# Kernel tuning notes

Measured on AMD Instinct MI355X. Metric: run time of the kernel, lower is better.

## Reference

```python
import jax, jax.numpy as jnp
import numpy as np

B, N, D_IN, D_H = 16, 8192, 64, 64
N_SUP, K_HOP = 2, 2
NUM_MAT = N_SUP * K_HOP + 1  # identity + k hops per support
D_CAT = D_IN + D_H


def setup_inputs() -> dict:
    key = jax.random.key(0)
    ks = jax.random.split(key, 6)
    inputs = jax.random.normal(ks[0], (B, N, D_IN), jnp.float32)
    states = jax.random.normal(ks[1], (B, N, D_H), jnp.float32)
    # random-walk-like supports: nonnegative, row mass ~O(1) so k-hop features stay sane
    supports = jax.random.uniform(ks[2], (N_SUP, N, N), jnp.float32) * (2.0 / N)
    W_ru = jax.random.normal(ks[3], (D_CAT * NUM_MAT, 2 * D_H), jnp.float32) * 0.02
    b_ru = jnp.ones((2 * D_H,), jnp.float32)  # bias_start=1.0
    W_c = jax.random.normal(ks[4], (D_CAT * NUM_MAT, D_H), jnp.float32) * 0.02
    b_c = jnp.zeros((D_H,), jnp.float32)
    return dict(inputs=inputs, states=states, supports=supports,
                W_ru=W_ru, b_ru=b_ru, W_c=W_c, b_c=b_c)


def _gconv(x, supports, W, b):
    # x: [B,N,D]; diffusion conv: concat [x, S x, (2 S - I applied via Chebyshev) ...]
    feats = [x]
    for i in range(N_SUP):
        s = supports[i]  # [N,N]
        x1 = jnp.einsum('nm,bmd->bnd', s, x)
        feats.append(x1)
        xk2, xk1 = x, x1
        for _ in range(2, K_HOP + 1):
            xk = 2.0 * jnp.einsum('nm,bmd->bnd', s, xk1) - xk2
            feats.append(xk)
            xk2, xk1 = xk1, xk
    h = jnp.concatenate(feats, axis=-1)  # [B,N,D*NUM_MAT]
    return jnp.einsum('bnf,fo->bno', h, W) + b


def reference(inputs, states, supports, W_ru, b_ru, W_c, b_c):
    x = jnp.concatenate([inputs, states], axis=-1)           # [B,N,D_CAT]
    ru = jax.nn.sigmoid(_gconv(x, supports, W_ru, b_ru))      # [B,N,2H]
    r, u = ru[..., :D_H], ru[..., D_H:]
    xc = jnp.concatenate([inputs, r * states], axis=-1)
    c = jnp.tanh(_gconv(xc, supports, W_c, b_c))              # [B,N,H]
    new_state = u * states + (1.0 - u) * c
    return new_state, new_state
```

## Files before the change

kernel.cpp:

```cpp
#include <hip/hip_runtime.h>
#include <math.h>

typedef unsigned short u16t;
typedef unsigned int   u32t;
using short8 = __attribute__((ext_vector_type(8))) short;
using f32x4  = __attribute__((ext_vector_type(4))) float;

#define SZ_S   67108864LL
#define SZ_F   16777216LL
#define SZ_G   8388608LL
#define OFF_S0  0LL
#define OFF_S1  67108864LL
#define OFF_XT  134217728LL
#define OFF_X10 150994944LL
#define OFF_Z0  167772160LL
#define OFF_X11 184549376LL
#define OFF_Z1  201326592LL
#define OFF_RUT 218103808LL
#define OFF_YT  234881024LL
#define OFF_Y10 243269632LL
#define OFF_ZY0 251658240LL
#define OFF_Y11 260046848LL
#define OFF_ZY1 268435456LL
#define OFF_CT  276824064LL
#define OFF_WRU 285212672LL
#define OFF_WC  285294592LL

__device__ __forceinline__ u16t f2b(float f) {
  u32t x = __float_as_uint(f);
  x += 0x7fffu + ((x >> 16) & 1u);
  return (u16t)(x >> 16);
}
__device__ __forceinline__ float b2f(u16t h) {
  return __uint_as_float(((u32t)h) << 16);
}
__device__ __forceinline__ void async16(const u16t* g, u16t* l) {
  __builtin_amdgcn_global_load_lds((const __attribute__((address_space(1))) void*)g,
                                   (__attribute__((address_space(3))) void*)l, 16, 0, 0);
}

__global__ void convert_s(const float* __restrict__ S, u16t* __restrict__ ws) {
  const long long tid = (long long)blockIdx.x * 256 + threadIdx.x;
  const float4* p = (const float4*)S;
  const float4 a = p[tid * 2];
  const float4 b = p[tid * 2 + 1];
  short8 o;
  o[0] = (short)f2b(a.x); o[1] = (short)f2b(a.y);
  o[2] = (short)f2b(a.z); o[3] = (short)f2b(a.w);
  o[4] = (short)f2b(b.x); o[5] = (short)f2b(b.y);
  o[6] = (short)f2b(b.z); o[7] = (short)f2b(b.w);
  *(short8*)&ws[OFF_S0 + tid * 8] = o;
}

__global__ void build_xt(const float* __restrict__ inputs,
                         const float* __restrict__ states,
                         u16t* __restrict__ ws) {
  __shared__ float tile[64][65];
  const int n0 = blockIdx.x * 64;
  const int half = blockIdx.y;
  const int b = blockIdx.z;
  const float* src = half ? states : inputs;
  const int t = threadIdx.x;
  const int d = t & 63, nl = t >> 6;
#pragma unroll
  for (int p = 0; p < 16; ++p) {
    const int n = p * 4 + nl;
    tile[d][n] = src[((long long)b * 8192 + n0 + n) * 64 + d];
  }
  __syncthreads();
  const int nn = t & 63, cl = t >> 6;
#pragma unroll
  for (int p = 0; p < 16; ++p) {
    const int c = p * 4 + cl;
    ws[OFF_XT + (long long)(b * 128 + half * 64 + c) * 8192 + n0 + nn] = f2b(tile[c][nn]);
  }
}

__global__ void prep_w(const float* __restrict__ Wru, const float* __restrict__ Wc,
                       u16t* __restrict__ ws) {
  const int t = blockIdx.x * 256 + threadIdx.x;
  if (t < 81920) {
    const int o = t / 640, f = t - o * 640;
    const int feat = f >> 7, dc = f & 127;
    float v;
    switch (feat) {
      case 0:  v = Wru[dc * 128 + o] - Wru[(256 + dc) * 128 + o] - Wru[(512 + dc) * 128 + o]; break;
      case 1:  v = Wru[(128 + dc) * 128 + o]; break;
      case 2:  v = 2.f * Wru[(256 + dc) * 128 + o]; break;
      case 3:  v = Wru[(384 + dc) * 128 + o]; break;
      default: v = 2.f * Wru[(512 + dc) * 128 + o]; break;
    }
    ws[OFF_WRU + t] = f2b(v);
  } else {
    const int t2 = t - 81920;
    const int o = t2 / 640, f = t2 - o * 640;
    const int feat = f >> 7, dc = f & 127;
    float v;
    switch (feat) {
      case 0:  v = Wc[dc * 64 + o] - Wc[(256 + dc) * 64 + o] - Wc[(512 + dc) * 64 + o]; break;
      case 1:  v = Wc[(128 + dc) * 64 + o]; break;
      case 2:  v = 2.f * Wc[(256 + dc) * 64 + o]; break;
      case 3:  v = Wc[(384 + dc) * 64 + o]; break;
      default: v = 2.f * Wc[(512 + dc) * 64 + o]; break;
    }
    ws[OFF_WC + t2] = f2b(v);
  }
}

__global__ __launch_bounds__(256, 2) void gemm_bt(const u16t* __restrict__ A,
                                                  const u16t* __restrict__ S,
                                                  u16t* __restrict__ Out) {
  __shared__ __align__(16) u16t As[128 * 64];
  __shared__ __align__(16) u16t Bs[128 * 64];
  const int t = threadIdx.x;
  const int l = t & 63;
  const int w = t >> 6;
  const int m0 = blockIdx.x * 128;
  const long long r0 = (long long)blockIdx.y * 128;

  const int srow = t >> 3;
  const int schunk = ((t & 7) ^ (srow & 7)) * 8;
  const u16t* ga = A + (r0 + srow) * 8192 + schunk;
  const u16t* gb = S + (long long)(m0 + srow) * 8192 + schunk;
  u16t* la = &As[t * 8];
  u16t* lb = &Bs[t * 8];

  f32x4 acc[4][4];
#pragma unroll
  for (int i = 0; i < 4; ++i)
#pragma unroll
    for (int j = 0; j < 4; ++j) acc[i][j] = f32x4{0.f, 0.f, 0.f, 0.f};

  const int wr = (w >> 1) * 64, wm = (w & 1) * 64;
  const int lm = l & 15, lq = l >> 4;

  for (int k0 = 0; k0 < 8192; k0 += 64) {
#pragma unroll
    for (int i = 0; i < 4; ++i) {
      async16(ga + (long long)i * 32 * 8192 + k0, la + i * 2048);
      async16(gb + (long long)i * 32 * 8192 + k0, lb + i * 2048);
    }
    __syncthreads();
#pragma unroll
    for (int s = 0; s < 2; ++s) {
      short8 af[4], bf[4];
      const int ch = s * 4 + lq;
#pragma unroll
      for (int i = 0; i < 4; ++i) {
        const int mr = wr + i * 16 + lm;
        const int nr = wm + i * 16 + lm;
        af[i] = *(const short8*)&As[mr * 64 + ((ch ^ (mr & 7)) * 8)];
        bf[i] = *(const short8*)&Bs[nr * 64 + ((ch ^ (nr & 7)) * 8)];
      }
#pragma unroll
      for (int i = 0; i < 4; ++i)
#pragma unroll
        for (int j = 0; j < 4; ++j)
          acc[i][j] = __builtin_amdgcn_mfma_f32_16x16x32_bf16(af[i], bf[j], acc[i][j], 0, 0, 0);
    }
    __syncthreads();
  }
#pragma unroll
  for (int i = 0; i < 4; ++i)
#pragma unroll
    for (int j = 0; j < 4; ++j)
#pragma unroll
      for (int rr = 0; rr < 4; ++rr) {
        const long long r = r0 + wr + i * 16 + lq * 4 + rr;
        const int c = m0 + wm + j * 16 + lm;
        Out[r * 8192 + c] = f2b(acc[i][j][rr]);
      }
}

__global__ __launch_bounds__(256, 2) void proj(const u16t* __restrict__ ws_c,
                                               u16t* __restrict__ ws_m,
                                               const float* __restrict__ bias,
                                               const int variant) {
  __shared__ __align__(16) u16t As[128 * 64];
  __shared__ __align__(16) u16t Bt[128 * 72];
  const long long FOFF[5] = {OFF_XT, OFF_X10, OFF_Z0, OFF_X11, OFF_Z1};
  const long long GOFF[5] = {OFF_YT, OFF_Y10, OFF_ZY0, OFF_Y11, OFF_ZY1};
  const int t = threadIdx.x;
  const int l = t & 63;
  const int w = t >> 6;
  const int n0 = blockIdx.x * 128;
  const int b = blockIdx.y;
  const u16t* Wt = ws_c + (variant ? OFF_WC : OFF_WRU);

  const int srow = t >> 3;
  const int schunk = ((t & 7) ^ (srow & 7)) * 8;
  const int wr = (w >> 1) * 64, wm = (w & 1) * 64;
  const int lm = l & 15, lq = l >> 4;

  f32x4 acc[4][4];
#pragma unroll
  for (int i = 0; i < 4; ++i)
#pragma unroll
    for (int j = 0; j < 4; ++j) acc[i][j] = f32x4{0.f, 0.f, 0.f, 0.f};

  for (int q = 0; q < 10; ++q) {
    const int feat = q >> 1, half = q & 1;
    long long brow;
    if (variant == 0)
      brow = FOFF[feat] + (long long)(b * 128 + half * 64) * 8192;
    else
      brow = half ? (GOFF[feat] + (long long)(b * 64) * 8192)
                  : (FOFF[feat] + (long long)(b * 128) * 8192);
#pragma unroll
    for (int i = 0; i < 4; ++i)
      async16(Wt + (i * 32 + srow) * 640 + q * 64 + schunk, &As[i * 2048 + t * 8]);
    const int fr = t >> 4;
    const int noff = (t & 15) * 8;
#pragma unroll
    for (int p = 0; p < 4; ++p) {
      const int f = p * 16 + fr;
      short8 v = *(const short8*)&ws_c[brow + (long long)f * 8192 + n0 + noff];
#pragma unroll
      for (int e = 0; e < 8; ++e) Bt[(noff + e) * 72 + f] = (u16t)v[e];
    }
    __syncthreads();
#pragma unroll
    for (int s = 0; s < 2; ++s) {
      short8 af[4], bf[4];
      const int ch = s * 4 + lq;
#pragma unroll
      for (int i = 0; i < 4; ++i) {
        const int mr = wr + i * 16 + lm;
        const int nr = wm + i * 16 + lm;
        af[i] = *(const short8*)&As[mr * 64 + ((ch ^ (mr & 7)) * 8)];
        bf[i] = *(const short8*)&Bt[nr * 72 + s * 32 + lq * 8];
      }
#pragma unroll
      for (int i = 0; i < 4; ++i)
#pragma unroll
        for (int j = 0; j < 4; ++j)
          acc[i][j] = __builtin_amdgcn_mfma_f32_16x16x32_bf16(af[i], bf[j], acc[i][j], 0, 0, 0);
    }
    __syncthreads();
  }

  if (variant == 0) {
#pragma unroll
    for (int i = 0; i < 4; ++i)
#pragma unroll
      for (int j = 0; j < 4; ++j)
#pragma unroll
        for (int rr = 0; rr < 4; ++rr) {
          const int o = wr + i * 16 + lq * 4 + rr;
          const int c = n0 + wm + j * 16 + lm;
          const float x = acc[i][j][rr] + bias[o];
          const float sg = 1.f / (1.f + __expf(-x));
          ws_m[OFF_RUT + (long long)(b * 128 + o) * 8192 + c] = f2b(sg);
        }
  } else if (wr == 0) {
#pragma unroll
    for (int i = 0; i < 4; ++i)
#pragma unroll
      for (int j = 0; j < 4; ++j)
#pragma unroll
        for (int rr = 0; rr < 4; ++rr) {
          const int o = i * 16 + lq * 4 + rr;
          const int c = n0 + wm + j * 16 + lm;
          const float x = acc[i][j][rr] + bias[o];
          ws_m[OFF_CT + (long long)(b * 64 + o) * 8192 + c] = f2b(tanhf(x));
        }
  }
}

__global__ void build_y(u16t* __restrict__ ws) {
  const long long tid = (long long)blockIdx.x * 256 + threadIdx.x;
  const int ry = (int)(tid >> 10);
  const int nc = ((int)tid & 1023) * 8;
  const int b = ry >> 6, d = ry & 63;
  const short8 r8 = *(const short8*)&ws[OFF_RUT + (long long)(b * 128 + d) * 8192 + nc];
  const short8 s8 = *(const short8*)&ws[OFF_XT + (long long)(b * 128 + 64 + d) * 8192 + nc];
  short8 o;
#pragma unroll
  for (int e = 0; e < 8; ++e) o[e] = (short)f2b(b2f((u16t)r8[e]) * b2f((u16t)s8[e]));
  *(short8*)&ws[OFF_YT + (long long)ry * 8192 + nc] = o;
}

__global__ void final_out(const u16t* __restrict__ ws,
                          const float* __restrict__ states,
                          float* __restrict__ out) {
  __shared__ float lu[64][65];
  __shared__ float lc[64][65];
  const int t = threadIdx.x;
  const int b = blockIdx.y;
  const int n0 = blockIdx.x * 64;
  const int dd = t >> 3, noff = (t & 7) * 8;
#pragma unroll
  for (int p = 0; p < 2; ++p) {
    const int d = p * 32 + dd;
    short8 u8 = *(const short8*)&ws[OFF_RUT + (long long)(b * 128 + 64 + d) * 8192 + n0 + noff];
    short8 c8 = *(const short8*)&ws[OFF_CT + (long long)(b * 64 + d) * 8192 + n0 + noff];
#pragma unroll
    for (int e = 0; e < 8; ++e) {
      lu[d][noff + e] = b2f((u16t)u8[e]);
      lc[d][noff + e] = b2f((u16t)c8[e]);
    }
  }
  __syncthreads();
  const int d = t & 63, nl = t >> 6;
#pragma unroll
  for (int p = 0; p < 16; ++p) {
    const int n = p * 4 + nl;
    const long long idx = ((long long)b * 8192 + n0 + n) * 64 + d;
    const float s = states[idx];
    const float u = lu[d][n];
    const float c = lc[d][n];
    const float v = u * s + (1.f - u) * c;
    out[idx] = v;
    out[idx + 8388608] = v;
  }
}

extern "C" void kernel_launch(void* const* d_in, const int* in_sizes, int n_in,
                              void* d_out, int out_size, void* d_ws, size_t ws_size,
                              hipStream_t stream) {
  (void)in_sizes; (void)n_in; (void)out_size; (void)ws_size;
  const float* inputs   = (const float*)d_in[0];
  const float* states   = (const float*)d_in[1];
  const float* supports = (const float*)d_in[2];
  const float* Wru      = (const float*)d_in[3];
  const float* bru      = (const float*)d_in[4];
  const float* Wc       = (const float*)d_in[5];
  const float* bc       = (const float*)d_in[6];
  u16t* ws = (u16t*)d_ws;
  float* out = (float*)d_out;

  convert_s<<<65536, 256, 0, stream>>>(supports, ws);
  build_xt<<<dim3(128, 2, 16), 256, 0, stream>>>(inputs, states, ws);
  prep_w<<<480, 256, 0, stream>>>(Wru, Wc, ws);

  gemm_bt<<<dim3(64, 16), 256, 0, stream>>>(ws + OFF_XT,  ws + OFF_S0, ws + OFF_X10);
  gemm_bt<<<dim3(64, 16), 256, 0, stream>>>(ws + OFF_X10, ws + OFF_S0, ws + OFF_Z0);
  gemm_bt<<<dim3(64, 16), 256, 0, stream>>>(ws + OFF_XT,  ws + OFF_S1, ws + OFF_X11);
  gemm_bt<<<dim3(64, 16), 256, 0, stream>>>(ws + OFF_X11, ws + OFF_S1, ws + OFF_Z1);

  proj<<<dim3(64, 16), 256, 0, stream>>>(ws, ws, bru, 0);
  build_y<<<4096, 256, 0, stream>>>(ws);

  gemm_bt<<<dim3(64, 8), 256, 0, stream>>>(ws + OFF_YT,  ws + OFF_S0, ws + OFF_Y10);
  gemm_bt<<<dim3(64, 8), 256, 0, stream>>>(ws + OFF_Y10, ws + OFF_S0, ws + OFF_ZY0);
  gemm_bt<<<dim3(64, 8), 256, 0, stream>>>(ws + OFF_YT,  ws + OFF_S1, ws + OFF_Y11);
  gemm_bt<<<dim3(64, 8), 256, 0, stream>>>(ws + OFF_Y11, ws + OFF_S1, ws + OFF_ZY1);

  proj<<<dim3(64, 16), 256, 0, stream>>>(ws, ws, bc, 1);
  final_out<<<dim3(128, 16), 256, 0, stream>>>(ws, states, out);
}
```

Before: 2.503 ms.

## Replace GEMM with 256x256 double-buffered pipelined kernel batching both supports

Swaps the 128x128 single-buffered GEMM for a 256x256-tile, 512-thread kernel. It double-buffers LDS, issues async global loads in half-tiles interleaved with MFMA phases, and uses explicit barriers, waitcnts and setprio to overlap loads with compute. Two supports run in one launch via blockIdx.z, and a grouped block-id swizzle is added for L2 reuse. The aim is to hide memory latency and raise arithmetic intensity per block. The cost is heavy register use (128 accumulator floats per thread), 128KB of LDS per block, and fragile manual wait counts.

```diff
diff --git a/kernel.cpp b/kernel.cpp
--- a/kernel.cpp
+++ b/kernel.cpp
@@ -107,68 +107,136 @@
   }
 }
 
-__global__ __launch_bounds__(256, 2) void gemm_bt(const u16t* __restrict__ A,
-                                                  const u16t* __restrict__ S,
-                                                  u16t* __restrict__ Out) {
-  __shared__ __align__(16) u16t As[128 * 64];
-  __shared__ __align__(16) u16t Bs[128 * 64];
+#define STAGE(g, lb, kt, half)                                                   \
+  { const long long kk2 = (long long)(((kt) & 127) * 64);                        \
+    async16((g) + ((long long)((half) * 128 + srl)) * 8192 + kk2 + ssx,          \
+            (lb) + (half) * 8192 + sld);                                         \
+    async16((g) + ((long long)((half) * 128 + srl + 8)) * 8192 + kk2 + ssx,      \
+            (lb) + (half) * 8192 + sld + 512); }
+
+#define GRP(T, CUR)                                                              \
+  {                                                                              \
+    short8 af0[8], af1[8], bf0[4], bf1[4];                                       \
+         \
+    _Pragma("unroll") for (int mi = 0; mi < 8; ++mi) {                           \
+      af0[mi] = *(const short8*)&As[CUR][ar0 + mi * 1024];                       \
+      af1[mi] = *(const short8*)&As[CUR][ar1 + mi * 1024];                       \
+    }                                                                            \
+    _Pragma("unroll") for (int nj = 0; nj < 4; ++nj)                             \
+      bf0[nj] = *(const short8*)&Bs[CUR][br0 + nj * 1024];                       \
+    STAGE(gB, Bs[1 - (CUR)], (T) + 1, 1);                                        \
+    __builtin_amdgcn_s_barrier();                                                \
+    asm volatile("s_waitcnt lgkmcnt(0)" ::: "memory");                           \
+    __builtin_amdgcn_sched_barrier(0);                                           \
+    __builtin_amdgcn_s_setprio(1);                                               \
+    _Pragma("unroll") for (int mi = 0; mi < 8; ++mi) {                           \
+      acc[mi][0] = __builtin_amdgcn_mfma_f32_16x16x32_bf16(af0[mi], bf0[0], acc[mi][0], 0, 0, 0); \
+      acc[mi][1] = __builtin_amdgcn_mfma_f32_16x16x32_bf16(af0[mi], bf0[1], acc[mi][1], 0, 0, 0); \
+    }                                                                            \
+    __builtin_amdgcn_s_setprio(0);                                               \
+    __builtin_amdgcn_s_barrier();                                                \
+       \
+    STAGE(gA, As[CUR], (T) + 2, 0);                                              \
+    __builtin_amdgcn_s_barrier();                                                \
+    __builtin_amdgcn_s_setprio(1);                                               \
+    _Pragma("unroll") for (int mi = 0; mi < 8; ++mi) {                           \
+      acc[mi][2] = __builtin_amdgcn_mfma_f32_16x16x32_bf16(af0[mi], bf0[2], acc[mi][2], 0, 0, 0); \
+      acc[mi][3] = __builtin_amdgcn_mfma_f32_16x16x32_bf16(af0[mi], bf0[3], acc[mi][3], 0, 0, 0); \
+    }                                                                            \
+    __builtin_amdgcn_s_setprio(0);                                               \
+    __builtin_amdgcn_s_barrier();                                                \
+                       \
+    _Pragma("unroll") for (int nj = 0; nj < 4; ++nj)                             \
+      bf1[nj] = *(const short8*)&Bs[CUR][br1 + nj * 1024];                       \
+    STAGE(gA, As[CUR], (T) + 2, 1);                                              \
+    __builtin_amdgcn_s_barrier();                                                \
+    asm volatile("s_waitcnt lgkmcnt(0)" ::: "memory");                           \
+    __builtin_amdgcn_sched_barrier(0);                                           \
+    __builtin_amdgcn_s_setprio(1);                                               \
+    _Pragma("unroll") for (int mi = 0; mi < 8; ++mi) {                           \
+      acc[mi][0] = __builtin_amdgcn_mfma_f32_16x16x32_bf16(af1[mi], bf1[0], acc[mi][0], 0, 0, 0); \
+      acc[mi][1] = __builtin_amdgcn_mfma_f32_16x16x32_bf16(af1[mi], bf1[1], acc[mi][1], 0, 0, 0); \
+    }                                                                            \
+    __builtin_amdgcn_s_setprio(0);                                               \
+    __builtin_amdgcn_s_barrier();                                                \
+       \
+    STAGE(gB, Bs[CUR], (T) + 2, 0);                                              \
+    __builtin_amdgcn_s_barrier();                                                \
+    __builtin_amdgcn_s_setprio(1);                                               \
+    _Pragma("unroll") for (int mi = 0; mi < 8; ++mi) {                           \
+      acc[mi][2] = __builtin_amdgcn_mfma_f32_16x16x32_bf16(af1[mi], bf1[2], acc[mi][2], 0, 0, 0); \
+      acc[mi][3] = __builtin_amdgcn_mfma_f32_16x16x32_bf16(af1[mi], bf1[3], acc[mi][3], 0, 0, 0); \
+    }                                                                            \
+    __builtin_amdgcn_s_setprio(0);                                               \
+    asm volatile("s_waitcnt vmcnt(6)" ::: "memory");                             \
+    __builtin_amdgcn_s_barrier();                                                \
+  }
+
+__global__ __launch_bounds__(512, 2) void gemm256(const u16t* __restrict__ Aa,
+                                                  const u16t* __restrict__ Sa,
+                                                  u16t* __restrict__ Oa,
+                                                  const u16t* __restrict__ Ab,
+                                                  const u16t* __restrict__ Sb,
+                                                  u16t* __restrict__ Ob) {
+  __shared__ __align__(16) u16t As[2][16384];
+  __shared__ __align__(16) u16t Bs[2][16384];
   const int t = threadIdx.x;
   const int l = t & 63;
   const int w = t >> 6;
-  const int m0 = blockIdx.x * 128;
-  const long long r0 = (long long)blockIdx.y * 128;
-
-  const int srow = t >> 3;
-  const int schunk = ((t & 7) ^ (srow & 7)) * 8;
-  const u16t* ga = A + (r0 + srow) * 8192 + schunk;
-  const u16t* gb = S + (long long)(m0 + srow) * 8192 + schunk;
-  u16t* la = &As[t * 8];
-  u16t* lb = &Bs[t * 8];
-
-  f32x4 acc[4][4];
-#pragma unroll
-  for (int i = 0; i < 4; ++i)
+  const int id = blockIdx.y * 32 + blockIdx.x;
+  const int cpx = (gridDim.y * 32) >> 3;
+  const int swz = (id & 7) * cpx + (id >> 3);
+  const int bx = swz & 31, by = swz >> 5;
+  const long long m0 = (long long)bx * 256;
+  const long long r0 = (long long)by * 256;
+  const u16t* A = blockIdx.z ? Ab : Aa;
+  const u16t* S = blockIdx.z ? Sb : Sa;
+  u16t* Out = blockIdx.z ? Ob : Oa;
+  const u16t* gA = A + r0 * 8192;
+  const u16t* gB = S + m0 * 8192;
+
+  const int wr = (w >> 2) * 128;
+  const int wc = (w & 3) * 64;
+  const int lm = l & 15, lq = l >> 4;
+
+  const int srl = w * 16 + (l >> 3);
+  const int ssx = ((l & 7) ^ ((l >> 3) & 7)) * 8;
+  const int sld = w * 1024 + l * 8;
+
+  const int ar0 = (wr + lm) * 64 + ((lq ^ (lm & 7)) * 8);
+  const int ar1 = (wr + lm) * 64 + (((4 + lq) ^ (lm & 7)) * 8);
+  const int br0 = (wc + lm) * 64 + ((lq ^ (lm & 7)) * 8);
+  const int br1 = (wc + lm) * 64 + (((4 + lq) ^ (lm & 7)) * 8);
+
+  f32x4 acc[8][4];
+#pragma unroll
+  for (int i = 0; i < 8; ++i)
 #pragma unroll
     for (int j = 0; j < 4; ++j) acc[i][j] = f32x4{0.f, 0.f, 0.f, 0.f};
 
-  const int wr = (w >> 1) * 64, wm = (w & 1) * 64;
-  const int lm = l & 15, lq = l >> 4;
-
-  for (int k0 = 0; k0 < 8192; k0 += 64) {
-#pragma unroll
-    for (int i = 0; i < 4; ++i) {
-      async16(ga + (long long)i * 32 * 8192 + k0, la + i * 2048);
-      async16(gb + (long long)i * 32 * 8192 + k0, lb + i * 2048);
-    }
-    __syncthreads();
-#pragma unroll
-    for (int s = 0; s < 2; ++s) {
-      short8 af[4], bf[4];
-      const int ch = s * 4 + lq;
-#pragma unroll
-      for (int i = 0; i < 4; ++i) {
-        const int mr = wr + i * 16 + lm;
-        const int nr = wm + i * 16 + lm;
-        af[i] = *(const short8*)&As[mr * 64 + ((ch ^ (mr & 7)) * 8)];
-        bf[i] = *(const short8*)&Bs[nr * 64 + ((ch ^ (nr & 7)) * 8)];
-      }
-#pragma unroll
-      for (int i = 0; i < 4; ++i)
-#pragma unroll
-        for (int j = 0; j < 4; ++j)
-          acc[i][j] = __builtin_amdgcn_mfma_f32_16x16x32_bf16(af[i], bf[j], acc[i][j], 0, 0, 0);
-    }
-    __syncthreads();
-  }
-#pragma unroll
-  for (int i = 0; i < 4; ++i)
-#pragma unroll
-    for (int j = 0; j < 4; ++j)
+  STAGE(gA, As[0], 0, 0); STAGE(gA, As[0], 0, 1);
+  STAGE(gB, Bs[0], 0, 0); STAGE(gB, Bs[0], 0, 1);
+  asm volatile("s_waitcnt vmcnt(4)" ::: "memory");
+  STAGE(gA, As[1], 1, 0); STAGE(gA, As[1], 1, 1);
+  STAGE(gB, Bs[1], 1, 0);
+  asm volatile("s_waitcnt vmcnt(6)" ::: "memory");
+  __builtin_amdgcn_s_barrier();
+
+#pragma unroll 1
+  for (int T = 0; T < 128; T += 2) {
+    GRP(T, 0)
+    GRP(T + 1, 1)
+  }
+
+#pragma unroll
+  for (int mi = 0; mi < 8; ++mi)
+#pragma unroll
+    for (int nj = 0; nj < 4; ++nj)
 #pragma unroll
       for (int rr = 0; rr < 4; ++rr) {
-        const long long r = r0 + wr + i * 16 + lq * 4 + rr;
-        const int c = m0 + wm + j * 16 + lm;
-        Out[r * 8192 + c] = f2b(acc[i][j][rr]);
+        const long long r = r0 + wr + mi * 16 + lq * 4 + rr;
+        const long long c = m0 + wc + nj * 16 + lm;
+        Out[r * 8192 + c] = f2b(acc[mi][nj][rr]);
       }
 }
 
@@ -333,18 +401,18 @@
   build_xt<<<dim3(128, 2, 16), 256, 0, stream>>>(inputs, states, ws);
   prep_w<<<480, 256, 0, stream>>>(Wru, Wc, ws);
 
-  gemm_bt<<<dim3(64, 16), 256, 0, stream>>>(ws + OFF_XT,  ws + OFF_S0, ws + OFF_X10);
-  gemm_bt<<<dim3(64, 16), 256, 0, stream>>>(ws + OFF_X10, ws + OFF_S0, ws + OFF_Z0);
-  gemm_bt<<<dim3(64, 16), 256, 0, stream>>>(ws + OFF_XT,  ws + OFF_S1, ws + OFF_X11);
-  gemm_bt<<<dim3(64, 16), 256, 0, stream>>>(ws + OFF_X11, ws + OFF_S1, ws + OFF_Z1);
+  gemm256<<<dim3(32, 8, 2), 512, 0, stream>>>(ws + OFF_XT,  ws + OFF_S0, ws + OFF_X10,
+                                              ws + OFF_XT,  ws + OFF_S1, ws + OFF_X11);
+  gemm256<<<dim3(32, 8, 2), 512, 0, stream>>>(ws + OFF_X10, ws + OFF_S0, ws + OFF_Z0,
+                                              ws + OFF_X11, ws + OFF_S1, ws + OFF_Z1);
 
   proj<<<dim3(64, 16), 256, 0, stream>>>(ws, ws, bru, 0);
   build_y<<<4096, 256, 0, stream>>>(ws);
 
-  gemm_bt<<<dim3(64, 8), 256, 0, stream>>>(ws + OFF_YT,  ws + OFF_S0, ws + OFF_Y10);
-  gemm_bt<<<dim3(64, 8), 256, 0, stream>>>(ws + OFF_Y10, ws + OFF_S0, ws + OFF_ZY0);
-  gemm_bt<<<dim3(64, 8), 256, 0, stream>>>(ws + OFF_YT,  ws + OFF_S1, ws + OFF_Y11);
-  gemm_bt<<<dim3(64, 8), 256, 0, stream>>>(ws + OFF_Y11, ws + OFF_S1, ws + OFF_ZY1);
+  gemm256<<<dim3(32, 4, 2), 512, 0, stream>>>(ws + OFF_YT,  ws + OFF_S0, ws + OFF_Y10,
+                                              ws + OFF_YT,  ws + OFF_S1, ws + OFF_Y11);
+  gemm256<<<dim3(32, 4, 2), 512, 0, stream>>>(ws + OFF_Y10, ws + OFF_S0, ws + OFF_ZY0,
+                                              ws + OFF_Y11, ws + OFF_S1, ws + OFF_ZY1);
 
   proj<<<dim3(64, 16), 256, 0, stream>>>(ws, ws, bc, 1);
   final_out<<<dim3(128, 16), 256, 0, stream>>>(ws, states, out);
```

Result: faster. 2.379 ms (-5.0%).

## Replace GEMM with 256x256-tile multi-stage pipelined kernel batching both supports

Applied to the files above, without the earlier changes.

Swaps the 128x128 single-buffered GEMM for a 256x256-tile, 512-thread kernel. It uses a 4-deep LDS ring of 32-wide K slices with async prefetch three steps ahead, register double-buffering of fragments, setprio around MFMA bursts, and a block-index swizzle for L2 locality. The two independent support GEMMs per hop are merged into one launch via blockIdx.z. The aim is to hide global-load latency, raise arithmetic intensity per LDS byte, and cut launch count, at the cost of much higher register and LDS pressure (128KB LDS with 2 blocks per CU requested).

```diff
diff --git a/kernel.cpp b/kernel.cpp
--- a/kernel.cpp
+++ b/kernel.cpp
@@ -107,68 +107,116 @@
   }
 }
 
-__global__ __launch_bounds__(256, 2) void gemm_bt(const u16t* __restrict__ A,
-                                                  const u16t* __restrict__ S,
-                                                  u16t* __restrict__ Out) {
-  __shared__ __align__(16) u16t As[128 * 64];
-  __shared__ __align__(16) u16t Bs[128 * 64];
+#define STAGE_A(kt, dst)                                                        \
+  { const long long kw = (long long)(((kt) & 255) * 32);                        \
+    async16(gA + (long long)srow2 * 8192 + kw + sgc8, (dst) + sldo);            \
+    async16(gA + (long long)(srow2 + 128) * 8192 + kw + sgc8, (dst) + 4096 + sldo); }
+#define STAGE_B(kt, dst)                                                        \
+  { const long long kw = (long long)(((kt) & 255) * 32);                        \
+    async16(gB + (long long)srow2 * 8192 + kw + sgc8, (dst) + 8192 + sldo);     \
+    async16(gB + (long long)(srow2 + 128) * 8192 + kw + sgc8, (dst) + 12288 + sldo); }
+
+__global__ __launch_bounds__(512, 2) void gemm256(const u16t* __restrict__ Aa,
+                                                  const u16t* __restrict__ Sa,
+                                                  u16t* __restrict__ Oa,
+                                                  const u16t* __restrict__ Ab,
+                                                  const u16t* __restrict__ Sb,
+                                                  u16t* __restrict__ Ob) {
+  __shared__ __align__(16) u16t lds[4][16384];
   const int t = threadIdx.x;
   const int l = t & 63;
   const int w = t >> 6;
-  const int m0 = blockIdx.x * 128;
-  const long long r0 = (long long)blockIdx.y * 128;
-
-  const int srow = t >> 3;
-  const int schunk = ((t & 7) ^ (srow & 7)) * 8;
-  const u16t* ga = A + (r0 + srow) * 8192 + schunk;
-  const u16t* gb = S + (long long)(m0 + srow) * 8192 + schunk;
-  u16t* la = &As[t * 8];
-  u16t* lb = &Bs[t * 8];
-
-  f32x4 acc[4][4];
-#pragma unroll
-  for (int i = 0; i < 4; ++i)
+  const int id = blockIdx.y * 32 + blockIdx.x;
+  const int cpx = (gridDim.y * 32) >> 3;
+  const int swz = (id & 7) * cpx + (id >> 3);
+  const int bx = swz & 31, by = swz >> 5;
+  const long long m0 = (long long)bx * 256;
+  const long long r0 = (long long)by * 256;
+  const u16t* A = blockIdx.z ? Ab : Aa;
+  const u16t* S = blockIdx.z ? Sb : Sa;
+  u16t* Out = blockIdx.z ? Ob : Oa;
+  const u16t* gA = A + r0 * 8192;
+  const u16t* gB = S + m0 * 8192;
+
+  const int wr = (w >> 2) * 128;
+  const int wc = (w & 3) * 64;
+  const int lm = l & 15, lq = l >> 4;
+
+  const int srow2 = t >> 2;
+  const int sgc8 = ((t & 3) ^ ((t >> 3) & 3)) * 8;
+  const int sldo = t * 8;
+
+  const int ch8 = (lq ^ ((lm >> 1) & 3)) * 8;
+  const int aoff = (wr + lm) * 32 + ch8;
+  const int boff0 = 8192 + (wc + lm) * 32 + ch8;
+  const int boff1 = boff0 + 1024;
+
+  f32x4 acc[8][4];
+#pragma unroll
+  for (int i = 0; i < 8; ++i)
 #pragma unroll
     for (int j = 0; j < 4; ++j) acc[i][j] = f32x4{0.f, 0.f, 0.f, 0.f};
 
-  const int wr = (w >> 1) * 64, wm = (w & 1) * 64;
-  const int lm = l & 15, lq = l >> 4;
-
-  for (int k0 = 0; k0 < 8192; k0 += 64) {
-#pragma unroll
-    for (int i = 0; i < 4; ++i) {
-      async16(ga + (long long)i * 32 * 8192 + k0, la + i * 2048);
-      async16(gb + (long long)i * 32 * 8192 + k0, lb + i * 2048);
-    }
-    __syncthreads();
-#pragma unroll
-    for (int s = 0; s < 2; ++s) {
-      short8 af[4], bf[4];
-      const int ch = s * 4 + lq;
-#pragma unroll
-      for (int i = 0; i < 4; ++i) {
-        const int mr = wr + i * 16 + lm;
-        const int nr = wm + i * 16 + lm;
-        af[i] = *(const short8*)&As[mr * 64 + ((ch ^ (mr & 7)) * 8)];
-        bf[i] = *(const short8*)&Bs[nr * 64 + ((ch ^ (nr & 7)) * 8)];
-      }
-#pragma unroll
-      for (int i = 0; i < 4; ++i)
-#pragma unroll
-        for (int j = 0; j < 4; ++j)
-          acc[i][j] = __builtin_amdgcn_mfma_f32_16x16x32_bf16(af[i], bf[j], acc[i][j], 0, 0, 0);
-    }
-    __syncthreads();
-  }
-#pragma unroll
-  for (int i = 0; i < 4; ++i)
-#pragma unroll
-    for (int j = 0; j < 4; ++j)
+  STAGE_A(0, &lds[0][0]); STAGE_B(0, &lds[0][0]);
+  STAGE_A(1, &lds[1][0]); STAGE_B(1, &lds[1][0]);
+  STAGE_A(2, &lds[2][0]); STAGE_B(2, &lds[2][0]);
+  asm volatile("s_waitcnt vmcnt(4)" ::: "memory");
+  __builtin_amdgcn_s_barrier();
+
+  short8 fa[8], fb[2], ga[8], gb[2];
+  {
+    const u16t* b0 = &lds[0][0];
+#pragma unroll
+    for (int mi = 0; mi < 8; ++mi) fa[mi] = *(const short8*)&b0[aoff + mi * 512];
+#pragma unroll
+    for (int j = 0; j < 2; ++j) fb[j] = *(const short8*)&b0[boff0 + j * 512];
+  }
+
+#pragma unroll 1
+  for (int T = 0; T < 256; ++T) {
+    const u16t* bT  = &lds[T & 3][0];
+    const u16t* bT1 = &lds[(T + 1) & 3][0];
+    u16t* sD = &lds[(T + 3) & 3][0];
+    STAGE_A(T + 3, sD);
+#pragma unroll
+    for (int mi = 0; mi < 8; ++mi) ga[mi] = *(const short8*)&bT[aoff + mi * 512];
+#pragma unroll
+    for (int j = 0; j < 2; ++j) gb[j] = *(const short8*)&bT[boff1 + j * 512];
+    __builtin_amdgcn_s_barrier();
+    __builtin_amdgcn_s_setprio(1);
+#pragma unroll
+    for (int mi = 0; mi < 8; ++mi) {
+      acc[mi][0] = __builtin_amdgcn_mfma_f32_16x16x32_bf16(fa[mi], fb[0], acc[mi][0], 0, 0, 0);
+      acc[mi][1] = __builtin_amdgcn_mfma_f32_16x16x32_bf16(fa[mi], fb[1], acc[mi][1], 0, 0, 0);
+    }
+    __builtin_amdgcn_s_setprio(0);
+    __builtin_amdgcn_s_barrier();
+    STAGE_B(T + 3, sD);
+#pragma unroll
+    for (int mi = 0; mi < 8; ++mi) fa[mi] = *(const short8*)&bT1[aoff + mi * 512];
+#pragma unroll
+    for (int j = 0; j < 2; ++j) fb[j] = *(const short8*)&bT1[boff0 + j * 512];
+    __builtin_amdgcn_s_barrier();
+    __builtin_amdgcn_s_setprio(1);
+#pragma unroll
+    for (int mi = 0; mi < 8; ++mi) {
+      acc[mi][2] = __builtin_amdgcn_mfma_f32_16x16x32_bf16(ga[mi], gb[0], acc[mi][2], 0, 0, 0);
+      acc[mi][3] = __builtin_amdgcn_mfma_f32_16x16x32_bf16(ga[mi], gb[1], acc[mi][3], 0, 0, 0);
+    }
+    __builtin_amdgcn_s_setprio(0);
+    asm volatile("s_waitcnt vmcnt(4)" ::: "memory");
+    __builtin_amdgcn_s_barrier();
+  }
+
+#pragma unroll
+  for (int mi = 0; mi < 8; ++mi)
+#pragma unroll
+    for (int nj = 0; nj < 4; ++nj)
 #pragma unroll
       for (int rr = 0; rr < 4; ++rr) {
-        const long long r = r0 + wr + i * 16 + lq * 4 + rr;
-        const int c = m0 + wm + j * 16 + lm;
-        Out[r * 8192 + c] = f2b(acc[i][j][rr]);
+        const long long r = r0 + wr + mi * 16 + lq * 4 + rr;
+        const long long c = m0 + wc + nj * 16 + lm;
+        Out[r * 8192 + c] = f2b(acc[mi][nj][rr]);
       }
 }
 
@@ -333,18 +381,18 @@
   build_xt<<<dim3(128, 2, 16), 256, 0, stream>>>(inputs, states, ws);
   prep_w<<<480, 256, 0, stream>>>(Wru, Wc, ws);
 
-  gemm_bt<<<dim3(64, 16), 256, 0, stream>>>(ws + OFF_XT,  ws + OFF_S0, ws + OFF_X10);
-  gemm_bt<<<dim3(64, 16), 256, 0, stream>>>(ws + OFF_X10, ws + OFF_S0, ws + OFF_Z0);
-  gemm_bt<<<dim3(64, 16), 256, 0, stream>>>(ws + OFF_XT,  ws + OFF_S1, ws + OFF_X11);
-  gemm_bt<<<dim3(64, 16), 256, 0, stream>>>(ws + OFF_X11, ws + OFF_S1, ws + OFF_Z1);
+  gemm256<<<dim3(32, 8, 2), 512, 0, stream>>>(ws + OFF_XT,  ws + OFF_S0, ws + OFF_X10,
+                                              ws + OFF_XT,  ws + OFF_S1, ws + OFF_X11);
+  gemm256<<<dim3(32, 8, 2), 512, 0, stream>>>(ws + OFF_X10, ws + OFF_S0, ws + OFF_Z0,
+                                              ws + OFF_X11, ws + OFF_S1, ws + OFF_Z1);
 
   proj<<<dim3(64, 16), 256, 0, stream>>>(ws, ws, bru, 0);
   build_y<<<4096, 256, 0, stream>>>(ws);
 
-  gemm_bt<<<dim3(64, 8), 256, 0, stream>>>(ws + OFF_YT,  ws + OFF_S0, ws + OFF_Y10);
-  gemm_bt<<<dim3(64, 8), 256, 0, stream>>>(ws + OFF_Y10, ws + OFF_S0, ws + OFF_ZY0);
-  gemm_bt<<<dim3(64, 8), 256, 0, stream>>>(ws + OFF_YT,  ws + OFF_S1, ws + OFF_Y11);
-  gemm_bt<<<dim3(64, 8), 256, 0, stream>>>(ws + OFF_Y11, ws + OFF_S1, ws + OFF_ZY1);
+  gemm256<<<dim3(32, 4, 2), 512, 0, stream>>>(ws + OFF_YT,  ws + OFF_S0, ws + OFF_Y10,
+                                              ws + OFF_YT,  ws + OFF_S1, ws + OFF_Y11);
+  gemm256<<<dim3(32, 4, 2), 512, 0, stream>>>(ws + OFF_Y10, ws + OFF_S0, ws + OFF_ZY0,
+                                              ws + OFF_Y11, ws + OFF_S1, ws + OFF_ZY1);
 
   proj<<<dim3(64, 16), 256, 0, stream>>>(ws, ws, bc, 1);
   final_out<<<dim3(128, 16), 256, 0, stream>>>(ws, states, out);
```

Measured after the change: 2.699 ms. 1.08x slower.
